# Kernel tuning notes

Hardware: AMD Instinct MI355X
Metric: run time of the kernel (lower is better)

Reference implementation:

```python
import jax, jax.numpy as jnp
import numpy as np

N, INPUTDIM, OUTDIM, GRIDSIZE = 32768, 64, 256, 32


def setup_inputs() -> dict:
    key = jax.random.key(0)
    k1, k2 = jax.random.split(key)
    x = jax.random.normal(k1, (N, INPUTDIM), dtype=jnp.float32)
    # xavier_uniform over tensor of shape (2, outdim, inputdim, gridsize):
    # fan_in = inputdim*gridsize, fan_out = outdim*gridsize (torch treats dim0=fan_out-ish,
    # but exact init scale is irrelevant for correctness; use a matching uniform range)
    fan_in = INPUTDIM * GRIDSIZE
    fan_out = OUTDIM * GRIDSIZE
    bound = float(np.sqrt(6.0 / (fan_in + fan_out)))
    fouriercoeffs = jax.random.uniform(
        k2, (2, OUTDIM, INPUTDIM, GRIDSIZE), dtype=jnp.float32,
        minval=-bound, maxval=bound)
    bias = jnp.zeros((1, OUTDIM), dtype=jnp.float32)
    return {"x": x, "fouriercoeffs": fouriercoeffs, "bias": bias}


def reference(x, fouriercoeffs, bias):
    # gridsize_param rounds back to GRIDSIZE at init -> static.
    g = fouriercoeffs.shape[-1]
    k = jnp.arange(1, g + 1, dtype=x.dtype)  # (g,)
    # Fourier feature expansion: (N, inputdim, g)
    xk = x[:, :, None] * k[None, None, :]
    c = jnp.cos(xk)
    s = jnp.sin(xk)
    # Contract over (inputdim, gridsize) -> two GEMMs over flattened dim
    y = jnp.einsum('nig,oig->no', c, fouriercoeffs[0])
    y = y + jnp.einsum('nig,oig->no', s, fouriercoeffs[1])
    y = y + bias  # (1, outdim) broadcasts over N
    return y
```

## Files before the change

kernel.cpp:

```cpp
#include <hip/hip_runtime.h>


#define IDIM 64
#define ODIM 256
#define KDIM 4096
#define BM 64
#define BN 256

typedef __attribute__((ext_vector_type(8))) unsigned short ushort8_t;
typedef __bf16 bf16x8 __attribute__((ext_vector_type(8)));
typedef float floatx4 __attribute__((ext_vector_type(4)));

__device__ __forceinline__ unsigned short f2bf_rne(float f) {
  unsigned int u = __float_as_uint(f);
  return (unsigned short)((u + 0x7FFFu + ((u >> 16) & 1u)) >> 16);
}

__device__ __forceinline__ void gl_lds16(const void* g, void* l) {
  __builtin_amdgcn_global_load_lds(
      (__attribute__((address_space(1))) void*)g,
      (__attribute__((address_space(3))) void*)l, 16, 0, 0);
}

__global__ void __launch_bounds__(256) wconv(const float* __restrict__ fc,
                                             unsigned short* __restrict__ Wr) {
  int e = (blockIdx.x * 256 + threadIdx.x) << 2;
  int o = e >> 12;
  int k = e & 4095;
  int i = k >> 6;
  int c = (k >> 5) & 1;
  int g = k & 31;
  const float4 v = *(const float4*)(fc + ((size_t)c << 19) + o * 2048 + i * 32 + g);
  ushort4 r;
  r.x = f2bf_rne(v.x);
  r.y = f2bf_rne(v.y);
  r.z = f2bf_rne(v.z);
  r.w = f2bf_rne(v.w);
  *(ushort4*)(Wr + e) = r;
}

__global__ void __launch_bounds__(256) fkan_gemm(const float* __restrict__ X,
                                                 const unsigned short* __restrict__ Wr,
                                                 const float* __restrict__ bias,
                                                 float* __restrict__ out) {
  __shared__ __align__(16) unsigned short As[2][BM * 64];
  __shared__ __align__(16) unsigned short Bs[2][BN * 64];

  const int t = threadIdx.x;
  const int wv = t >> 6;
  const int ln = t & 63;
  const int lm = ln & 15;
  const int quad = ln >> 4;
  const int wn = wv;
  const int m0 = blockIdx.y * BM;

  const int arow = t >> 2;
  const int q = t & 3;
  const float g0f = (float)(8 * q + 1);

  const int brow_off = ln >> 3;
  const int bchunk = (ln & 7) ^ (ln >> 3);
  const unsigned short* bbase =
      Wr + (size_t)(wv * 64 + brow_off) * KDIM + bchunk * 8;

  const int ga_c = arow * 8 + (q ^ (arow & 7));
  const int ga_s = arow * 8 + ((4 + q) ^ (arow & 7));

  floatx4 acc[4][4];
#pragma unroll
  for (int a = 0; a < 4; ++a)
#pragma unroll
    for (int b = 0; b < 4; ++b)
      acc[a][b] = (floatx4){0.0f, 0.0f, 0.0f, 0.0f};

  const float* xptr = X + (size_t)(m0 + arow) * IDIM;

  auto stageB = [&](int ktn, int buf) {
#pragma unroll
    for (int j = 0; j < 8; ++j) {
      gl_lds16(bbase + (size_t)j * 8 * KDIM + ktn * 64,
               &Bs[buf][(wv * 8 + j) * 512]);
    }
  };

  auto features = [&](float xv, int buf) {
    const float inv2pi = 0.15915494309189535f;
    float u = xv * inv2pi;
    float u0 = u * g0f;
    float c1 = __builtin_amdgcn_cosf(u);
    float s1 = __builtin_amdgcn_sinf(u);
    float C = __builtin_amdgcn_cosf(u0);
    float S = __builtin_amdgcn_sinf(u0);
    bf16x8 cb, sb;
    cb[0] = (__bf16)C;
    sb[0] = (__bf16)S;
#pragma unroll
    for (int j = 1; j < 8; ++j) {
      float Cn = __builtin_fmaf(C, c1, -(S * s1));
      float Sn = __builtin_fmaf(S, c1, (C * s1));
      C = Cn;
      S = Sn;
      cb[j] = (__bf16)C;
      sb[j] = (__bf16)S;
    }
    ushort8_t* As8 = (ushort8_t*)As[buf];
    As8[ga_c] = __builtin_bit_cast(ushort8_t, cb);
    As8[ga_s] = __builtin_bit_cast(ushort8_t, sb);
  };

  auto domfma = [&](int buf) {
#pragma unroll
    for (int kh = 0; kh < 2; ++kh) {
      bf16x8 af[4], bfr[4];
#pragma unroll
      for (int mt = 0; mt < 4; ++mt) {
        int r = mt * 16 + lm;
        int gran = r * 8 + ((kh * 4 + quad) ^ (r & 7));
        af[mt] = __builtin_bit_cast(bf16x8, ((const ushort8_t*)As[buf])[gran]);
      }
#pragma unroll
      for (int nt = 0; nt < 4; ++nt) {
        int n = wn * 64 + nt * 16 + lm;
        int gran = n * 8 + ((kh * 4 + quad) ^ (n & 7));
        bfr[nt] = __builtin_bit_cast(bf16x8, ((const ushort8_t*)Bs[buf])[gran]);
      }
#pragma unroll
      for (int mt = 0; mt < 4; ++mt)
#pragma unroll
        for (int nt = 0; nt < 4; ++nt)
          acc[mt][nt] = __builtin_amdgcn_mfma_f32_16x16x32_bf16(
              af[mt], bfr[nt], acc[mt][nt], 0, 0, 0);
    }
  };

  stageB(0, 0);
  features(xptr[0], 0);
  __syncthreads();

  for (int kt = 0; kt < 62; kt += 2) {
    {
      float xn = xptr[kt + 1];
      stageB(kt + 1, 1);
      domfma(0);
      features(xn, 1);
      __syncthreads();
    }
    {
      float xn = xptr[kt + 2];
      stageB(kt + 2, 0);
      domfma(1);
      features(xn, 0);
      __syncthreads();
    }
  }
  {
    float xn = xptr[63];
    stageB(63, 1);
    domfma(0);
    features(xn, 1);
    __syncthreads();
  }
  domfma(1);

#pragma unroll
  for (int nt = 0; nt < 4; ++nt) {
    int col = wn * 64 + nt * 16 + lm;
    float bv = bias[col];
#pragma unroll
    for (int mt = 0; mt < 4; ++mt) {
      int rbase = m0 + mt * 16 + quad * 4;
#pragma unroll
      for (int r = 0; r < 4; ++r)
        out[(size_t)(rbase + r) * ODIM + col] = acc[mt][nt][r] + bv;
    }
  }
}

extern "C" void kernel_launch(void* const* d_in, const int* in_sizes, int n_in,
                              void* d_out, int out_size, void* d_ws, size_t ws_size,
                              hipStream_t stream) {
  const float* x = (const float*)d_in[0];
  const float* fc = (const float*)d_in[1];
  const float* bias = (const float*)d_in[2];
  float* out = (float*)d_out;
  unsigned short* Wr = (unsigned short*)d_ws;

  hipLaunchKernelGGL(wconv, dim3(1024), dim3(256), 0, stream, fc, Wr);
  hipLaunchKernelGGL(fkan_gemm, dim3(1, 512), dim3(256), 0, stream, x, Wr, bias, out);
}
```

Baseline: 149.8 us.

## Double M tile to 128 with 512-thread blocks and intra-block split-K reduction

Raises the block tile to 128 rows, uses 512 threads (8 waves), and splits each K-tile's two halves across wave pairs, each computing a 64x128 subtile. The partial sums are then reduced through shared memory before bias is added and results stored. This halves the number of B-tile (weight) loads per output row and gives each wave a larger MFMA tile for better operand reuse. In exchange it adds a reduction epilogue with extra barriers, 96KB of LDS, and higher register pressure from 32 accumulators, which may limit occupancy.

```diff
diff --git a/kernel.cpp b/kernel.cpp
--- a/kernel.cpp
+++ b/kernel.cpp
@@ -4,8 +4,7 @@
 #define IDIM 64
 #define ODIM 256
 #define KDIM 4096
-#define BM 64
-#define BN 256
+#define BM 128
 
 typedef __attribute__((ext_vector_type(8))) unsigned short ushort8_t;
 typedef __bf16 bf16x8 __attribute__((ext_vector_type(8)));
@@ -39,20 +38,23 @@
   *(ushort4*)(Wr + e) = r;
 }
 
-__global__ void __launch_bounds__(256) fkan_gemm(const float* __restrict__ X,
-                                                 const unsigned short* __restrict__ Wr,
-                                                 const float* __restrict__ bias,
-                                                 float* __restrict__ out) {
-  __shared__ __align__(16) unsigned short As[2][BM * 64];
-  __shared__ __align__(16) unsigned short Bs[2][BN * 64];
+__global__ void __launch_bounds__(512, 2) fkan_gemm(const float* __restrict__ X,
+                                                    const unsigned short* __restrict__ Wr,
+                                                    const float* __restrict__ bias,
+                                                    float* __restrict__ out) {
+  __shared__ __align__(16) unsigned char smem[98304];
+  unsigned short* const AsBase = (unsigned short*)smem;
+  unsigned short* const BsBase = (unsigned short*)(smem + 32768);
 
   const int t = threadIdx.x;
   const int wv = t >> 6;
   const int ln = t & 63;
   const int lm = ln & 15;
   const int quad = ln >> 4;
-  const int wn = wv;
-  const int m0 = blockIdx.y * BM;
+  const int wk = wv & 1;
+  const int wn2 = (wv >> 1) & 1;
+  const int wm2 = wv >> 2;
+  const int m0 = blockIdx.x * BM;
 
   const int arow = t >> 2;
   const int q = t & 3;
@@ -60,27 +62,27 @@
 
   const int brow_off = ln >> 3;
   const int bchunk = (ln & 7) ^ (ln >> 3);
-  const unsigned short* bbase =
-      Wr + (size_t)(wv * 64 + brow_off) * KDIM + bchunk * 8;
+  const unsigned short* bsrc[4];
+#pragma unroll
+  for (int j = 0; j < 4; ++j)
+    bsrc[j] = Wr + (size_t)(wv * 32 + j * 8 + brow_off) * KDIM + bchunk * 8;
 
   const int ga_c = arow * 8 + (q ^ (arow & 7));
   const int ga_s = arow * 8 + ((4 + q) ^ (arow & 7));
 
-  floatx4 acc[4][4];
+  floatx4 acc[4][8];
 #pragma unroll
   for (int a = 0; a < 4; ++a)
 #pragma unroll
-    for (int b = 0; b < 4; ++b)
+    for (int b = 0; b < 8; ++b)
       acc[a][b] = (floatx4){0.0f, 0.0f, 0.0f, 0.0f};
 
   const float* xptr = X + (size_t)(m0 + arow) * IDIM;
 
   auto stageB = [&](int ktn, int buf) {
 #pragma unroll
-    for (int j = 0; j < 8; ++j) {
-      gl_lds16(bbase + (size_t)j * 8 * KDIM + ktn * 64,
-               &Bs[buf][(wv * 8 + j) * 512]);
-    }
+    for (int j = 0; j < 4; ++j)
+      gl_lds16(bsrc[j] + ktn * 64, BsBase + buf * 16384 + (wv * 4 + j) * 512);
   };
 
   auto features = [&](float xv, int buf) {
@@ -103,34 +105,32 @@
       cb[j] = (__bf16)C;
       sb[j] = (__bf16)S;
     }
-    ushort8_t* As8 = (ushort8_t*)As[buf];
+    ushort8_t* As8 = (ushort8_t*)(AsBase + buf * 8192);
     As8[ga_c] = __builtin_bit_cast(ushort8_t, cb);
     As8[ga_s] = __builtin_bit_cast(ushort8_t, sb);
   };
 
   auto domfma = [&](int buf) {
-#pragma unroll
-    for (int kh = 0; kh < 2; ++kh) {
-      bf16x8 af[4], bfr[4];
-#pragma unroll
-      for (int mt = 0; mt < 4; ++mt) {
-        int r = mt * 16 + lm;
-        int gran = r * 8 + ((kh * 4 + quad) ^ (r & 7));
-        af[mt] = __builtin_bit_cast(bf16x8, ((const ushort8_t*)As[buf])[gran]);
-      }
-#pragma unroll
-      for (int nt = 0; nt < 4; ++nt) {
-        int n = wn * 64 + nt * 16 + lm;
-        int gran = n * 8 + ((kh * 4 + quad) ^ (n & 7));
-        bfr[nt] = __builtin_bit_cast(bf16x8, ((const ushort8_t*)Bs[buf])[gran]);
-      }
-#pragma unroll
-      for (int mt = 0; mt < 4; ++mt)
-#pragma unroll
-        for (int nt = 0; nt < 4; ++nt)
-          acc[mt][nt] = __builtin_amdgcn_mfma_f32_16x16x32_bf16(
-              af[mt], bfr[nt], acc[mt][nt], 0, 0, 0);
-    }
+    const ushort8_t* A8 = (const ushort8_t*)(AsBase + buf * 8192);
+    const ushort8_t* B8 = (const ushort8_t*)(BsBase + buf * 16384);
+    const int ch = wk * 4 + quad;
+    bf16x8 af[4], bfr[8];
+#pragma unroll
+    for (int mt = 0; mt < 4; ++mt) {
+      int r = wm2 * 64 + mt * 16 + lm;
+      af[mt] = __builtin_bit_cast(bf16x8, A8[r * 8 + (ch ^ (r & 7))]);
+    }
+#pragma unroll
+    for (int nt = 0; nt < 8; ++nt) {
+      int n = wn2 * 128 + nt * 16 + lm;
+      bfr[nt] = __builtin_bit_cast(bf16x8, B8[n * 8 + (ch ^ (n & 7))]);
+    }
+#pragma unroll
+    for (int mt = 0; mt < 4; ++mt)
+#pragma unroll
+      for (int nt = 0; nt < 8; ++nt)
+        acc[mt][nt] = __builtin_amdgcn_mfma_f32_16x16x32_bf16(
+            af[mt], bfr[nt], acc[mt][nt], 0, 0, 0);
   };
 
   stageB(0, 0);
@@ -162,16 +162,35 @@
   }
   domfma(1);
 
-#pragma unroll
-  for (int nt = 0; nt < 4; ++nt) {
-    int col = wn * 64 + nt * 16 + lm;
-    float bv = bias[col];
-#pragma unroll
-    for (int mt = 0; mt < 4; ++mt) {
-      int rbase = m0 + mt * 16 + quad * 4;
-#pragma unroll
-      for (int r = 0; r < 4; ++r)
-        out[(size_t)(rbase + r) * ODIM + col] = acc[mt][nt][r] + bv;
+  float* red = (float*)smem;
+  for (int half = 0; half < 2; ++half) {
+    __syncthreads();
+    if (wk == 1 && wm2 == half) {
+#pragma unroll
+      for (int mt = 0; mt < 4; ++mt)
+#pragma unroll
+        for (int nt = 0; nt < 8; ++nt) {
+          int col = wn2 * 128 + nt * 16 + lm;
+#pragma unroll
+          for (int idx = 0; idx < 4; ++idx)
+            red[(mt * 16 + quad * 4 + idx) * 260 + col] = acc[mt][nt][idx];
+        }
+    }
+    __syncthreads();
+    if (wk == 0 && wm2 == half) {
+#pragma unroll
+      for (int nt = 0; nt < 8; ++nt) {
+        int col = wn2 * 128 + nt * 16 + lm;
+        float bv = bias[col];
+#pragma unroll
+        for (int mt = 0; mt < 4; ++mt) {
+          int rbase = m0 + half * 64 + mt * 16 + quad * 4;
+#pragma unroll
+          for (int idx = 0; idx < 4; ++idx)
+            out[(size_t)(rbase + idx) * ODIM + col] =
+                acc[mt][nt][idx] + red[(mt * 16 + quad * 4 + idx) * 260 + col] + bv;
+        }
+      }
     }
   }
 }
@@ -186,5 +205,5 @@
   unsigned short* Wr = (unsigned short*)d_ws;
 
   hipLaunchKernelGGL(wconv, dim3(1024), dim3(256), 0, stream, fc, Wr);
-  hipLaunchKernelGGL(fkan_gemm, dim3(1, 512), dim3(256), 0, stream, x, Wr, bias, out);
-}
+  hipLaunchKernelGGL(fkan_gemm, dim3(256), dim3(512), 0, stream, x, Wr, bias, out);
+}
```

Result: faster. 138.9 us (-7.3%).
